# Kernel tuning notes

Measured on AMD Instinct MI355X. Metric: run time of the kernel, lower is better.

Reference implementation:

```python
import jax, jax.numpy as jnp
import numpy as np

HEAD_DIM = 64
N_HEADS = 32
N_KV = 8
ROPE_BASE = 500000.0
FREQ_CONFIG = {"factor": 32.0, "low_freq_factor": 1.0, "high_freq_factor": 4.0, "original_context_length": 8192}


def _rope_tables(head_dim, theta, n_pos, fc):
    # faithful to precompute_rope_params with llama3 freq scaling
    inv_freq = 1.0 / theta ** (np.arange(0, head_dim, 2, dtype=np.float32) / head_dim)
    low_wl = fc["original_context_length"] / fc["low_freq_factor"]
    high_wl = fc["original_context_length"] / fc["high_freq_factor"]
    wavelen = 2.0 * np.pi / inv_freq
    inv_l = np.where(wavelen > low_wl, inv_freq / fc["factor"], inv_freq)
    smooth = (fc["original_context_length"] / wavelen - fc["low_freq_factor"]) / (fc["high_freq_factor"] - fc["low_freq_factor"])
    smoothed = (1.0 - smooth) * (inv_freq / fc["factor"]) + smooth * inv_freq
    med = (wavelen <= low_wl) & (wavelen >= high_wl)
    inv_freq = np.where(med, smoothed, inv_l)
    pos = np.arange(n_pos, dtype=np.float32)
    angles = pos[:, None] * inv_freq[None, :]          # [T, head_dim/2]
    angles = np.concatenate([angles, angles], axis=1)  # [T, head_dim]
    return jnp.asarray(np.cos(angles), jnp.float32), jnp.asarray(np.sin(angles), jnp.float32)


def _apply_rope(x, cos, sin):
    # x: [b, h, t, d]; cos/sin: [t, d]
    d = x.shape[-1]
    x1, x2 = x[..., : d // 2], x[..., d // 2:]
    rotated = jnp.concatenate([-x2, x1], axis=-1)
    return x * cos[None, None] + rotated * sin[None, None]


def setup_inputs() -> dict:
    key = jax.random.key(0)
    ks = jax.random.split(key, 5)
    b, t, d = 1, 2048, 2048
    s = 0.02
    return {
        "x": jax.random.normal(ks[0], (b, t, d), jnp.float32),
        "Wq": jax.random.normal(ks[1], (d, d), jnp.float32) * s,
        "Wk": jax.random.normal(ks[2], (N_KV * HEAD_DIM, d), jnp.float32) * s,
        "Wv": jax.random.normal(ks[3], (N_KV * HEAD_DIM, d), jnp.float32) * s,
        "Wo": jax.random.normal(ks[4], (d, d), jnp.float32) * s,
        "start_pos": 0,
    }


def reference(x, Wq, Wk, Wv, Wo, start_pos):
    b, t, _ = x.shape
    cos, sin = _rope_tables(HEAD_DIM, ROPE_BASE, start_pos + t, FREQ_CONFIG)
    cos, sin = cos[start_pos:start_pos + t], sin[start_pos:start_pos + t]

    q = (x @ Wq.T).reshape(b, t, N_HEADS, HEAD_DIM).transpose(0, 2, 1, 3)  # [b,H,t,d]
    k = (x @ Wk.T).reshape(b, t, N_KV, HEAD_DIM).transpose(0, 2, 1, 3)     # [b,G,t,d]
    v = (x @ Wv.T).reshape(b, t, N_KV, HEAD_DIM).transpose(0, 2, 1, 3)

    q = _apply_rope(q, cos, sin)
    k = _apply_rope(k, cos, sin)

    n_rep = N_HEADS // N_KV
    k = jnp.repeat(k, n_rep, axis=1)  # [b,H,t,d]
    v = jnp.repeat(v, n_rep, axis=1)

    scores = jnp.einsum("bhqd,bhkd->bhqk", q, k)
    causal = jnp.triu(jnp.ones((t, t), bool), k=1)
    scores = jnp.where(causal[None, None], -jnp.inf, scores) / jnp.sqrt(jnp.float32(HEAD_DIM))
    weights = jax.nn.softmax(scores, axis=-1)
    ctx = jnp.einsum("bhqk,bhkd->bhqd", weights, v)
    ctx = ctx.transpose(0, 2, 1, 3).reshape(b, t, N_HEADS * HEAD_DIM)
    return ctx @ Wo.T
```

## Files before the change

### kernel.cpp

```cpp
#include <hip/hip_runtime.h>
#include <math.h>

#define T_SEQ 2048
#define D_MODEL 2048
#define HEAD_DIM 64
#define N_HEADS 32
#define N_KV 8

using short8 = __attribute__((ext_vector_type(8))) short;
using f32x4  = __attribute__((ext_vector_type(4))) float;
using f32x16 = __attribute__((ext_vector_type(16))) float;
using u32x4  = __attribute__((ext_vector_type(4))) unsigned int;

#define MFMA16(a, b, c) __builtin_amdgcn_mfma_f32_16x16x32_bf16(a, b, c, 0, 0, 0)
#define MFMA32(a, b, c) __builtin_amdgcn_mfma_f32_32x32x16_bf16(a, b, c, 0, 0, 0)

__device__ __forceinline__ unsigned short f2bf(float f) {
    unsigned int u = __builtin_bit_cast(unsigned int, f);
    u += 0x7fff + ((u >> 16) & 1);
    return (unsigned short)(u >> 16);
}
__device__ __forceinline__ void gld_lds16(const ushort* g, ushort* l) {
    __builtin_amdgcn_global_load_lds((const __attribute__((address_space(1))) void*)g,
                                     (__attribute__((address_space(3))) void*)l, 16, 0, 0);
}
__device__ __forceinline__ unsigned int cvtpk(float lo, float hi) {
    unsigned int r;
    asm("v_cvt_pk_bf16_f32 %0, %1, %2" : "=v"(r) : "v"(lo), "v"(hi));
    return r;
}
__device__ __forceinline__ void plswap(unsigned int& a, unsigned int& b) {
    auto r = __builtin_amdgcn_permlane32_swap(a, b, false, false);
    a = r[0];
    b = r[1];
}

__global__ __launch_bounds__(256) void rope_tables_kernel(float* __restrict__ cosT, float* __restrict__ sinT,
                                                          const int* __restrict__ start_pos, int T) {
    int idx = blockIdx.x * 256 + threadIdx.x;
    int t = idx >> 5;
    int i = idx & 31;
    float pos = (float)(start_pos[0] + t);
    float expo = (float)i / 32.0f;
    float inv_freq = 1.0f / powf(500000.0f, expo);
    const float two_pi = 6.283185307179586f;
    float wavelen = two_pi / inv_freq;
    const float low_wl = 8192.0f;
    const float high_wl = 2048.0f;
    float inv;
    if (wavelen > low_wl) {
        inv = inv_freq / 32.0f;
    } else if (wavelen < high_wl) {
        inv = inv_freq;
    } else {
        float smooth = (8192.0f / wavelen - 1.0f) / 3.0f;
        inv = (1.0f - smooth) * (inv_freq / 32.0f) + smooth * inv_freq;
    }
    float ang = pos * inv;
    cosT[i * T + t] = cosf(ang);
    sinT[i * T + t] = sinf(ang);
}

__global__ __launch_bounds__(256) void cast_all_kernel(
    const float* __restrict__ x, const float* __restrict__ wq,
    const float* __restrict__ wk, const float* __restrict__ wv,
    const float* __restrict__ wo,
    ushort* __restrict__ xb, ushort* __restrict__ wqb,
    ushort* __restrict__ wkb, ushort* __restrict__ wvb, ushort* __restrict__ wob) {
    int i = blockIdx.x * 256 + threadIdx.x;
    const float* src; ushort* dst; int off;
    if (i < 1048576)      { src = x;  dst = xb;  off = i; }
    else if (i < 2097152) { src = wq; dst = wqb; off = i - 1048576; }
    else if (i < 2359296) { src = wk; dst = wkb; off = i - 2097152; }
    else if (i < 2621440) { src = wv; dst = wvb; off = i - 2359296; }
    else                  { src = wo; dst = wob; off = i - 2621440; }
    float4 v = ((const float4*)src)[off];
    ushort4 o;
    o.x = f2bf(v.x); o.y = f2bf(v.y); o.z = f2bf(v.z); o.w = f2bf(v.w);
    ((ushort4*)dst)[off] = o;
}

__global__ __launch_bounds__(256) void gemm_qkv(
    const ushort* __restrict__ X, const ushort* __restrict__ Wqb,
    const ushort* __restrict__ Wkb, const ushort* __restrict__ Wvb,
    ushort* __restrict__ Qo, ushort* __restrict__ Ko, ushort* __restrict__ Vto,
    const float* __restrict__ cosT, const float* __restrict__ sinT,
    int T, int D) {
    __shared__ __align__(16) ushort As[2][2][2048];
    __shared__ __align__(16) ushort Bs[2][2][4096];
    const int tid = threadIdx.x;
    const int w = tid >> 6, l = tid & 63;
    const int m0 = blockIdx.x * 64;
    const int n0g = blockIdx.y * 128;

    const ushort* B;
    ushort* Cout;
    int n0, doRope;
    if (n0g < 2048)      { B = Wqb + (size_t)n0g * D;          Cout = Qo;  n0 = n0g;        doRope = 1; }
    else if (n0g < 2560) { B = Wkb + (size_t)(n0g - 2048) * D; Cout = Ko;  n0 = n0g - 2048; doRope = 1; }
    else                 { B = Wvb + (size_t)(n0g - 2560) * D; Cout = Vto; n0 = n0g - 2560; doRope = 0; }

    const int wm = (w >> 1) * 32, wn = (w & 1) * 64;
    const int lr = l & 15;
    const int quad = l >> 4;

    f32x4 zero = {0.f, 0.f, 0.f, 0.f};
    f32x4 acc[2][4];
#pragma unroll
    for (int i = 0; i < 2; ++i)
#pragma unroll
        for (int j = 0; j < 4; ++j) acc[i][j] = zero;

    const int srow = l >> 2;
    const int scg  = ((l & 3) ^ (srow & 3)) * 8;
    const ushort* Ag  = X + (size_t)(m0 + 16 * w + srow) * D + scg;
    const ushort* Bg0 = B + (size_t)(16 * (2 * w) + srow) * D + scg;
    const ushort* Bg1 = B + (size_t)(16 * (2 * w + 1) + srow) * D + scg;

#define GSTAGE(k0v, nb) { \
    gld_lds16(Ag  + (k0v),      &As[nb][0][w * 512]); \
    gld_lds16(Ag  + (k0v) + 32, &As[nb][1][w * 512]); \
    gld_lds16(Bg0 + (k0v),      &Bs[nb][0][(2 * w) * 512]); \
    gld_lds16(Bg0 + (k0v) + 32, &Bs[nb][1][(2 * w) * 512]); \
    gld_lds16(Bg1 + (k0v),      &Bs[nb][0][(2 * w + 1) * 512]); \
    gld_lds16(Bg1 + (k0v) + 32, &Bs[nb][1][(2 * w + 1) * 512]); }

    GSTAGE(0, 0);

    const int rsw = (quad ^ (lr & 3)) * 8;
    for (int k0 = 0; k0 < D; k0 += 64) {
        const int b = (k0 >> 6) & 1;
        __syncthreads();
        if (k0 + 64 < D) GSTAGE(k0 + 64, b ^ 1);
#pragma unroll
        for (int sub = 0; sub < 2; ++sub) {
            short8 af[2], bf[4];
#pragma unroll
            for (int i = 0; i < 2; ++i) af[i] = *(const short8*)&As[b][sub][(wm + i * 16 + lr) * 32 + rsw];
#pragma unroll
            for (int j = 0; j < 4; ++j) bf[j] = *(const short8*)&Bs[b][sub][(wn + j * 16 + lr) * 32 + rsw];
#pragma unroll
            for (int i = 0; i < 2; ++i)
#pragma unroll
                for (int j = 0; j < 4; ++j)
                    acc[i][j] = MFMA16(af[i], bf[j], acc[i][j]);
        }
    }
#undef GSTAGE

    const int mbase = m0 + wm + quad * 4;
    if (doRope) {
        const float qsc = (n0g < 2048) ? 0.18033688011112042f : 1.0f;
#pragma unroll
        for (int i = 0; i < 2; ++i) {
            int trow = mbase + i * 16;
#pragma unroll
            for (int j = 0; j < 2; ++j) {
                int i1 = lr + j * 16;
                float4 c4 = *(const float4*)&cosT[(size_t)i1 * T + trow];
                float4 s4 = *(const float4*)&sinT[(size_t)i1 * T + trow];
                int n1 = n0 + wn + lr + j * 16;
                int n2 = n1 + 32;
                size_t b1 = (size_t)(n1 >> 6) * ((size_t)T * 64) + (size_t)(n1 & 63);
                size_t b2 = (size_t)(n2 >> 6) * ((size_t)T * 64) + (size_t)(n2 & 63);
                float cs[4] = {c4.x, c4.y, c4.z, c4.w};
                float sn[4] = {s4.x, s4.y, s4.z, s4.w};
#pragma unroll
                for (int r = 0; r < 4; ++r) {
                    float x1 = acc[i][j][r], x2 = acc[i][j + 2][r];
                    Cout[b1 + (size_t)(trow + r) * 64] = f2bf((x1 * cs[r] - x2 * sn[r]) * qsc);
                    Cout[b2 + (size_t)(trow + r) * 64] = f2bf((x2 * cs[r] + x1 * sn[r]) * qsc);
                }
            }
        }
    } else {
#pragma unroll
        for (int i = 0; i < 2; ++i)
#pragma unroll
            for (int j = 0; j < 4; ++j) {
                int n = n0 + wn + lr + j * 16;
                int m = mbase + i * 16;
                ushort4 o;
                o.x = f2bf(acc[i][j][0]); o.y = f2bf(acc[i][j][1]);
                o.z = f2bf(acc[i][j][2]); o.w = f2bf(acc[i][j][3]);
                *(ushort4*)&Vto[(size_t)n * T + m] = o;
            }
    }
}

__global__ __launch_bounds__(256) void gemm_bt_f32(const ushort* __restrict__ A,
                                                   const ushort* __restrict__ B,
                                                   float* __restrict__ C,
                                                   int M, int N, int K) {
    __shared__ __align__(16) ushort As[2][2][2048];
    __shared__ __align__(16) ushort Bs[2][2][4096];
    const int tid = threadIdx.x;
    const int w = tid >> 6, l = tid & 63;
    const int m0 = blockIdx.x * 64, n0 = blockIdx.y * 128;
    const int wm = (w >> 1) * 32, wn = (w & 1) * 64;
    const int lr = l & 15;
    const int quad = l >> 4;

    f32x4 zero = {0.f, 0.f, 0.f, 0.f};
    f32x4 acc[2][4];
#pragma unroll
    for (int i = 0; i < 2; ++i)
#pragma unroll
        for (int j = 0; j < 4; ++j) acc[i][j] = zero;

    const int srow = l >> 2;
    const int scg  = ((l & 3) ^ (srow & 3)) * 8;
    const ushort* Ag  = A + (size_t)(m0 + 16 * w + srow) * K + scg;
    const ushort* Bg0 = B + (size_t)(n0 + 16 * (2 * w) + srow) * K + scg;
    const ushort* Bg1 = B + (size_t)(n0 + 16 * (2 * w + 1) + srow) * K + scg;

#define GSTAGE(k0v, nb) { \
    gld_lds16(Ag  + (k0v),      &As[nb][0][w * 512]); \
    gld_lds16(Ag  + (k0v) + 32, &As[nb][1][w * 512]); \
    gld_lds16(Bg0 + (k0v),      &Bs[nb][0][(2 * w) * 512]); \
    gld_lds16(Bg0 + (k0v) + 32, &Bs[nb][1][(2 * w) * 512]); \
    gld_lds16(Bg1 + (k0v),      &Bs[nb][0][(2 * w + 1) * 512]); \
    gld_lds16(Bg1 + (k0v) + 32, &Bs[nb][1][(2 * w + 1) * 512]); }

    GSTAGE(0, 0);

    const int rsw = (quad ^ (lr & 3)) * 8;
    for (int k0 = 0; k0 < K; k0 += 64) {
        const int b = (k0 >> 6) & 1;
        __syncthreads();
        if (k0 + 64 < K) GSTAGE(k0 + 64, b ^ 1);
#pragma unroll
        for (int sub = 0; sub < 2; ++sub) {
            short8 af[2], bf[4];
#pragma unroll
            for (int i = 0; i < 2; ++i) af[i] = *(const short8*)&As[b][sub][(wm + i * 16 + lr) * 32 + rsw];
#pragma unroll
            for (int j = 0; j < 4; ++j) bf[j] = *(const short8*)&Bs[b][sub][(wn + j * 16 + lr) * 32 + rsw];
#pragma unroll
            for (int i = 0; i < 2; ++i)
#pragma unroll
                for (int j = 0; j < 4; ++j)
                    acc[i][j] = MFMA16(af[i], bf[j], acc[i][j]);
        }
    }
#undef GSTAGE

    const int mbase = m0 + wm + quad * 4;
    const int nbase = n0 + wn + lr;
#pragma unroll
    for (int i = 0; i < 2; ++i)
#pragma unroll
        for (int j = 0; j < 4; ++j)
#pragma unroll
            for (int r = 0; r < 4; ++r)
                C[(size_t)(mbase + i * 16 + r) * N + (nbase + j * 16)] = acc[i][j][r];
}

__global__ __launch_bounds__(128, 2) void attn_mfma(const ushort* __restrict__ Q,
                                                    const ushort* __restrict__ K,
                                                    const ushort* __restrict__ Vt,
                                                    ushort* __restrict__ ctx, int T) {
    __shared__ __align__(16) ushort Ks[2][4096];
    __shared__ __align__(16) ushort Vs[2][4096];
    const int tid = threadIdx.x, w = tid >> 6, l = tid & 63;
    const int lq = l & 31, hi = l >> 5;
    const int h = blockIdx.y, hk = h >> 2;
    const int qb = ((h >> 3) & 1) ? (31 - (int)blockIdx.x) : (int)blockIdx.x;
    const int ntiles = qb + 1;
    const ushort* Kb = K + (size_t)hk * T * 64;
    const ushort* Vb = Vt + (size_t)hk * 64 * T;

    const int srow = l >> 3;
    const int sc   = ((l & 7) ^ srow) * 8;

    const ushort* Qrow = Q + ((size_t)h * T + qb * 64 + w * 32 + lq) * 64;
    short8 qf[4];
#pragma unroll
    for (int ks = 0; ks < 4; ++ks)
        qf[ks] = *(const short8*)(Qrow + ks * 16 + hi * 8);

    f32x16 oacc0, oacc1;
#pragma unroll
    for (int r = 0; r < 16; ++r) { oacc0[r] = 0.f; oacc1[r] = 0.f; }
    float ls[4] = {0.f, 0.f, 0.f, 0.f};
    const int limit = w * 32 + lq;

#define ASTAGE(kt, buf) do { \
    size_t _k0 = (size_t)(kt) * 64; \
    const int _s0 = w * 4; \
    gld_lds16(Kb + (_k0 + _s0 * 8      + srow) * 64 + sc, &Ks[buf][(_s0    ) * 512]); \
    gld_lds16(Kb + (_k0 + _s0 * 8 + 8  + srow) * 64 + sc, &Ks[buf][(_s0 + 1) * 512]); \
    gld_lds16(Kb + (_k0 + _s0 * 8 + 16 + srow) * 64 + sc, &Ks[buf][(_s0 + 2) * 512]); \
    gld_lds16(Kb + (_k0 + _s0 * 8 + 24 + srow) * 64 + sc, &Ks[buf][(_s0 + 3) * 512]); \
    gld_lds16(Vb + (size_t)(_s0 * 8      + srow) * T + _k0 + sc, &Vs[buf][(_s0    ) * 512]); \
    gld_lds16(Vb + (size_t)(_s0 * 8 + 8  + srow) * T + _k0 + sc, &Vs[buf][(_s0 + 1) * 512]); \
    gld_lds16(Vb + (size_t)(_s0 * 8 + 16 + srow) * T + _k0 + sc, &Vs[buf][(_s0 + 2) * 512]); \
    gld_lds16(Vb + (size_t)(_s0 * 8 + 24 + srow) * T + _k0 + sc, &Vs[buf][(_s0 + 3) * 512]); \
} while (0)

    ASTAGE(0, 0);

    for (int kt = 0; kt < ntiles; ++kt) {
        const int b = kt & 1;
        __syncthreads();
        if (kt + 1 < ntiles) ASTAGE(kt + 1, b ^ 1);

        f32x16 s0, s1;
#pragma unroll
        for (int r = 0; r < 16; ++r) { s0[r] = 0.f; s1[r] = 0.f; }
#pragma unroll
        for (int ks = 0; ks < 4; ++ks) {
            const int c = ((ks * 2 + hi) ^ (lq & 7)) * 8;
            short8 kf0 = *(const short8*)&Ks[b][lq * 64 + c];
            short8 kf1 = *(const short8*)&Ks[b][(lq + 32) * 64 + c];
            s0 = MFMA32(kf0, qf[ks], s0);
            s1 = MFMA32(kf1, qf[ks], s1);
        }

        f32x16 p0, p1;
        if (kt == ntiles - 1) {
#pragma unroll
            for (int r = 0; r < 16; ++r) {
                const int kk = (r & 3) + 8 * (r >> 2) + 4 * hi;
                p0[r] = (kk <= limit)      ? __builtin_amdgcn_exp2f(s0[r]) : 0.f;
                p1[r] = (kk + 32 <= limit) ? __builtin_amdgcn_exp2f(s1[r]) : 0.f;
            }
        } else {
#pragma unroll
            for (int r = 0; r < 16; ++r) {
                p0[r] = __builtin_amdgcn_exp2f(s0[r]);
                p1[r] = __builtin_amdgcn_exp2f(s1[r]);
            }
        }
#pragma unroll
        for (int r = 0; r < 16; ++r) ls[r & 3] += p0[r] + p1[r];

#pragma unroll
        for (int ks2 = 0; ks2 < 4; ++ks2) {
            const f32x16& pp = (ks2 < 2) ? p0 : p1;
            const int bse = (ks2 & 1) * 8;
            unsigned int a0 = cvtpk(pp[bse + 0], pp[bse + 1]);
            unsigned int a1 = cvtpk(pp[bse + 2], pp[bse + 3]);
            unsigned int b0 = cvtpk(pp[bse + 4], pp[bse + 5]);
            unsigned int b1 = cvtpk(pp[bse + 6], pp[bse + 7]);
            plswap(a0, b0);
            plswap(a1, b1);
            u32x4 tw = {a0, a1, b0, b1};
            short8 pf = __builtin_bit_cast(short8, tw);
            const int c = ((ks2 * 2 + hi) ^ (lq & 7)) * 8;
            short8 vf0 = *(const short8*)&Vs[b][lq * 64 + c];
            short8 vf1 = *(const short8*)&Vs[b][(lq + 32) * 64 + c];
            oacc0 = MFMA32(vf0, pf, oacc0);
            oacc1 = MFMA32(vf1, pf, oacc1);
        }
    }
#undef ASTAGE

    float vsum = (ls[0] + ls[1]) + (ls[2] + ls[3]);
    vsum += __shfl_xor(vsum, 32, 64);
    const float inv = 1.f / vsum;

    ushort* cp = ctx + (size_t)(qb * 64 + w * 32 + lq) * 2048 + h * 64;
#pragma unroll
    for (int g = 0; g < 4; ++g) {
        ushort4 o0, o1;
        o0.x = f2bf(oacc0[4 * g + 0] * inv); o0.y = f2bf(oacc0[4 * g + 1] * inv);
        o0.z = f2bf(oacc0[4 * g + 2] * inv); o0.w = f2bf(oacc0[4 * g + 3] * inv);
        *(ushort4*)&cp[g * 8 + hi * 4] = o0;
        o1.x = f2bf(oacc1[4 * g + 0] * inv); o1.y = f2bf(oacc1[4 * g + 1] * inv);
        o1.z = f2bf(oacc1[4 * g + 2] * inv); o1.w = f2bf(oacc1[4 * g + 3] * inv);
        *(ushort4*)&cp[32 + g * 8 + hi * 4] = o1;
    }
}

extern "C" void kernel_launch(void* const* d_in, const int* in_sizes, int n_in,
                              void* d_out, int out_size, void* d_ws, size_t ws_size,
                              hipStream_t stream) {
    const float* x  = (const float*)d_in[0];
    const float* Wq = (const float*)d_in[1];
    const float* Wk = (const float*)d_in[2];
    const float* Wv = (const float*)d_in[3];
    const float* Wo = (const float*)d_in[4];
    const int* start_pos = (const int*)d_in[5];
    float* out = (float*)d_out;

    const int T = T_SEQ, D = D_MODEL;
    const int KV = N_KV * HEAD_DIM;

    char* w = (char*)d_ws;
    float* cosT = (float*)w;            w += (size_t)32 * T * 4;
    float* sinT = (float*)w;            w += (size_t)32 * T * 4;
    ushort* xbf  = (ushort*)w;          w += (size_t)T * D * 2;
    ushort* wqbf = (ushort*)w;          w += (size_t)D * D * 2;
    ushort* wkbf = (ushort*)w;          w += (size_t)KV * D * 2;
    ushort* wvbf = (ushort*)w;          w += (size_t)KV * D * 2;
    ushort* wobf = (ushort*)w;          w += (size_t)D * D * 2;
    ushort* qbf  = (ushort*)w;          w += (size_t)N_HEADS * T * 64 * 2;
    ushort* kbf  = (ushort*)w;          w += (size_t)N_KV * T * 64 * 2;
    ushort* vtbf = (ushort*)w;          w += (size_t)N_KV * 64 * T * 2;
    ushort* ctxbf = xbf;

    rope_tables_kernel<<<dim3((T * 32) / 256), dim3(256), 0, stream>>>(cosT, sinT, start_pos, T);

    cast_all_kernel<<<dim3(14336), dim3(256), 0, stream>>>(x, Wq, Wk, Wv, Wo,
                                                           xbf, wqbf, wkbf, wvbf, wobf);

    gemm_qkv<<<dim3(T / 64, (D + 2 * KV) / 128), dim3(256), 0, stream>>>(
        xbf, wqbf, wkbf, wvbf, qbf, kbf, vtbf, cosT, sinT, T, D);

    attn_mfma<<<dim3(32, N_HEADS), dim3(128), 0, stream>>>(qbf, kbf, vtbf, ctxbf, T);

    gemm_bt_f32<<<dim3(T / 64, D / 128), dim3(256), 0, stream>>>(ctxbf, wobf, out, T, D, D);
}
```

Before: 205.4 us.

## Use single-wave attention blocks loading K/V directly from global memory

The attention kernel moves from two-wave blocks that share double-buffered LDS tiles of K/V to single-wave blocks of 32 query rows. Each wave reads K and V fragments straight from global memory (relying on cache) with no LDS and no barriers. It also skips the fully masked half of the last tile, launches blocks heaviest-first, and raises wave priority around the MFMA sections. The cost is twice as many global K/V fetches per query row and exposed load latency, since nothing is prefetched.

```diff
diff --git a/kernel.cpp b/kernel.cpp
--- a/kernel.cpp
+++ b/kernel.cpp
@@ -256,87 +256,86 @@
                 C[(size_t)(mbase + i * 16 + r) * N + (nbase + j * 16)] = acc[i][j][r];
 }
 
-__global__ __launch_bounds__(128, 2) void attn_mfma(const ushort* __restrict__ Q,
-                                                    const ushort* __restrict__ K,
-                                                    const ushort* __restrict__ Vt,
-                                                    ushort* __restrict__ ctx, int T) {
-    __shared__ __align__(16) ushort Ks[2][4096];
-    __shared__ __align__(16) ushort Vs[2][4096];
-    const int tid = threadIdx.x, w = tid >> 6, l = tid & 63;
+__global__ __launch_bounds__(64, 4) void attn_mfma(const ushort* __restrict__ Q,
+                                                   const ushort* __restrict__ K,
+                                                   const ushort* __restrict__ Vt,
+                                                   ushort* __restrict__ ctx, int T) {
+    const int l = threadIdx.x;
     const int lq = l & 31, hi = l >> 5;
     const int h = blockIdx.y, hk = h >> 2;
-    const int qb = ((h >> 3) & 1) ? (31 - (int)blockIdx.x) : (int)blockIdx.x;
-    const int ntiles = qb + 1;
+    const int qt = 63 - (int)blockIdx.x;
+    const int ntiles = qt / 2 + 1;
+    const int qrow = qt * 32 + lq;
     const ushort* Kb = K + (size_t)hk * T * 64;
     const ushort* Vb = Vt + (size_t)hk * 64 * T;
 
-    const int srow = l >> 3;
-    const int sc   = ((l & 7) ^ srow) * 8;
-
-    const ushort* Qrow = Q + ((size_t)h * T + qb * 64 + w * 32 + lq) * 64;
+    const ushort* Qrow = Q + ((size_t)h * T + qrow) * 64;
     short8 qf[4];
 #pragma unroll
     for (int ks = 0; ks < 4; ++ks)
         qf[ks] = *(const short8*)(Qrow + ks * 16 + hi * 8);
 
+    const ushort* Kl = Kb + (size_t)lq * 64 + hi * 8;
+    const ushort* Vl = Vb + (size_t)lq * T + hi * 8;
+
     f32x16 oacc0, oacc1;
 #pragma unroll
     for (int r = 0; r < 16; ++r) { oacc0[r] = 0.f; oacc1[r] = 0.f; }
     float ls[4] = {0.f, 0.f, 0.f, 0.f};
-    const int limit = w * 32 + lq;
-
-#define ASTAGE(kt, buf) do { \
-    size_t _k0 = (size_t)(kt) * 64; \
-    const int _s0 = w * 4; \
-    gld_lds16(Kb + (_k0 + _s0 * 8      + srow) * 64 + sc, &Ks[buf][(_s0    ) * 512]); \
-    gld_lds16(Kb + (_k0 + _s0 * 8 + 8  + srow) * 64 + sc, &Ks[buf][(_s0 + 1) * 512]); \
-    gld_lds16(Kb + (_k0 + _s0 * 8 + 16 + srow) * 64 + sc, &Ks[buf][(_s0 + 2) * 512]); \
-    gld_lds16(Kb + (_k0 + _s0 * 8 + 24 + srow) * 64 + sc, &Ks[buf][(_s0 + 3) * 512]); \
-    gld_lds16(Vb + (size_t)(_s0 * 8      + srow) * T + _k0 + sc, &Vs[buf][(_s0    ) * 512]); \
-    gld_lds16(Vb + (size_t)(_s0 * 8 + 8  + srow) * T + _k0 + sc, &Vs[buf][(_s0 + 1) * 512]); \
-    gld_lds16(Vb + (size_t)(_s0 * 8 + 16 + srow) * T + _k0 + sc, &Vs[buf][(_s0 + 2) * 512]); \
-    gld_lds16(Vb + (size_t)(_s0 * 8 + 24 + srow) * T + _k0 + sc, &Vs[buf][(_s0 + 3) * 512]); \
-} while (0)
-
-    ASTAGE(0, 0);
 
     for (int kt = 0; kt < ntiles; ++kt) {
-        const int b = kt & 1;
-        __syncthreads();
-        if (kt + 1 < ntiles) ASTAGE(kt + 1, b ^ 1);
+        const int k0 = kt * 64;
+        const bool last = (kt == ntiles - 1);
+        const bool halfT = last && ((qt & 1) == 0);
 
         f32x16 s0, s1;
 #pragma unroll
         for (int r = 0; r < 16; ++r) { s0[r] = 0.f; s1[r] = 0.f; }
+        __builtin_amdgcn_s_setprio(1);
 #pragma unroll
         for (int ks = 0; ks < 4; ++ks) {
-            const int c = ((ks * 2 + hi) ^ (lq & 7)) * 8;
-            short8 kf0 = *(const short8*)&Ks[b][lq * 64 + c];
-            short8 kf1 = *(const short8*)&Ks[b][(lq + 32) * 64 + c];
+            short8 kf0 = *(const short8*)(Kl + (size_t)(k0) * 64 + ks * 16);
             s0 = MFMA32(kf0, qf[ks], s0);
-            s1 = MFMA32(kf1, qf[ks], s1);
-        }
+        }
+        if (!halfT) {
+#pragma unroll
+            for (int ks = 0; ks < 4; ++ks) {
+                short8 kf1 = *(const short8*)(Kl + (size_t)(k0 + 32) * 64 + ks * 16);
+                s1 = MFMA32(kf1, qf[ks], s1);
+            }
+        }
+        __builtin_amdgcn_s_setprio(0);
 
         f32x16 p0, p1;
-        if (kt == ntiles - 1) {
+        if (last) {
 #pragma unroll
             for (int r = 0; r < 16; ++r) {
-                const int kk = (r & 3) + 8 * (r >> 2) + 4 * hi;
-                p0[r] = (kk <= limit)      ? __builtin_amdgcn_exp2f(s0[r]) : 0.f;
-                p1[r] = (kk + 32 <= limit) ? __builtin_amdgcn_exp2f(s1[r]) : 0.f;
+                const int kk = k0 + (r & 3) + 8 * (r >> 2) + 4 * hi;
+                p0[r] = (kk <= qrow) ? __builtin_amdgcn_exp2f(s0[r]) : 0.f;
+            }
+            if (!halfT) {
+#pragma unroll
+                for (int r = 0; r < 16; ++r) {
+                    const int kk = k0 + 32 + (r & 3) + 8 * (r >> 2) + 4 * hi;
+                    p1[r] = (kk <= qrow) ? __builtin_amdgcn_exp2f(s1[r]) : 0.f;
+                }
             }
         } else {
 #pragma unroll
-            for (int r = 0; r < 16; ++r) {
-                p0[r] = __builtin_amdgcn_exp2f(s0[r]);
-                p1[r] = __builtin_amdgcn_exp2f(s1[r]);
-            }
-        }
-#pragma unroll
-        for (int r = 0; r < 16; ++r) ls[r & 3] += p0[r] + p1[r];
-
-#pragma unroll
-        for (int ks2 = 0; ks2 < 4; ++ks2) {
+            for (int r = 0; r < 16; ++r) p0[r] = __builtin_amdgcn_exp2f(s0[r]);
+#pragma unroll
+            for (int r = 0; r < 16; ++r) p1[r] = __builtin_amdgcn_exp2f(s1[r]);
+        }
+#pragma unroll
+        for (int r = 0; r < 16; ++r) ls[r & 3] += p0[r];
+        if (!halfT) {
+#pragma unroll
+            for (int r = 0; r < 16; ++r) ls[r & 3] += p1[r];
+        }
+
+        const int nks2 = halfT ? 2 : 4;
+        __builtin_amdgcn_s_setprio(1);
+        for (int ks2 = 0; ks2 < nks2; ++ks2) {
             const f32x16& pp = (ks2 < 2) ? p0 : p1;
             const int bse = (ks2 & 1) * 8;
             unsigned int a0 = cvtpk(pp[bse + 0], pp[bse + 1]);
@@ -347,20 +346,19 @@
             plswap(a1, b1);
             u32x4 tw = {a0, a1, b0, b1};
             short8 pf = __builtin_bit_cast(short8, tw);
-            const int c = ((ks2 * 2 + hi) ^ (lq & 7)) * 8;
-            short8 vf0 = *(const short8*)&Vs[b][lq * 64 + c];
-            short8 vf1 = *(const short8*)&Vs[b][(lq + 32) * 64 + c];
+            short8 vf0 = *(const short8*)(Vl + k0 + ks2 * 16);
+            short8 vf1 = *(const short8*)(Vl + (size_t)32 * T + k0 + ks2 * 16);
             oacc0 = MFMA32(vf0, pf, oacc0);
             oacc1 = MFMA32(vf1, pf, oacc1);
         }
-    }
-#undef ASTAGE
+        __builtin_amdgcn_s_setprio(0);
+    }
 
     float vsum = (ls[0] + ls[1]) + (ls[2] + ls[3]);
     vsum += __shfl_xor(vsum, 32, 64);
     const float inv = 1.f / vsum;
 
-    ushort* cp = ctx + (size_t)(qb * 64 + w * 32 + lq) * 2048 + h * 64;
+    ushort* cp = ctx + (size_t)qrow * 2048 + h * 64;
 #pragma unroll
     for (int g = 0; g < 4; ++g) {
         ushort4 o0, o1;
@@ -408,7 +406,7 @@
     gemm_qkv<<<dim3(T / 64, (D + 2 * KV) / 128), dim3(256), 0, stream>>>(
         xbf, wqbf, wkbf, wvbf, qbf, kbf, vtbf, cosT, sinT, T, D);
 
-    attn_mfma<<<dim3(32, N_HEADS), dim3(128), 0, stream>>>(qbf, kbf, vtbf, ctxbf, T);
+    attn_mfma<<<dim3(64, N_HEADS), dim3(64), 0, stream>>>(qbf, kbf, vtbf, ctxbf, T);
 
     gemm_bt_f32<<<dim3(T / 64, D / 128), dim3(256), 0, stream>>>(ctxbf, wobf, out, T, D, D);
 }
```

Measured after the change: 290.3 us. 41.3% more time.

## Share KV tiles across head pairs in attention and fuse rope-table into cast kernel

Applied to the files above, without the earlier changes.

The attention kernel now runs 256-thread blocks that cover two query heads sharing one KV head, so each K/V tile staged in LDS serves both heads. It also stages two 64-key tiles per step, which halves the number of barriers. Causal masking on the last tile skips the upper half of the score and PV MFMAs for the first row group, and s_setprio is raised around the MFMA sections. Separately, the rope-table computation is folded into the cast kernel as extra blocks, which removes one launch. The cost is more LDS per block (32KB) and added control-flow complexity.

```diff
diff --git a/kernel.cpp b/kernel.cpp
--- a/kernel.cpp
+++ b/kernel.cpp
@@ -35,38 +35,37 @@
     b = r[1];
 }
 
-__global__ __launch_bounds__(256) void rope_tables_kernel(float* __restrict__ cosT, float* __restrict__ sinT,
-                                                          const int* __restrict__ start_pos, int T) {
-    int idx = blockIdx.x * 256 + threadIdx.x;
-    int t = idx >> 5;
-    int i = idx & 31;
-    float pos = (float)(start_pos[0] + t);
-    float expo = (float)i / 32.0f;
-    float inv_freq = 1.0f / powf(500000.0f, expo);
-    const float two_pi = 6.283185307179586f;
-    float wavelen = two_pi / inv_freq;
-    const float low_wl = 8192.0f;
-    const float high_wl = 2048.0f;
-    float inv;
-    if (wavelen > low_wl) {
-        inv = inv_freq / 32.0f;
-    } else if (wavelen < high_wl) {
-        inv = inv_freq;
-    } else {
-        float smooth = (8192.0f / wavelen - 1.0f) / 3.0f;
-        inv = (1.0f - smooth) * (inv_freq / 32.0f) + smooth * inv_freq;
-    }
-    float ang = pos * inv;
-    cosT[i * T + t] = cosf(ang);
-    sinT[i * T + t] = sinf(ang);
-}
-
-__global__ __launch_bounds__(256) void cast_all_kernel(
+__global__ __launch_bounds__(256) void cast_rope_kernel(
     const float* __restrict__ x, const float* __restrict__ wq,
     const float* __restrict__ wk, const float* __restrict__ wv,
     const float* __restrict__ wo,
     ushort* __restrict__ xb, ushort* __restrict__ wqb,
-    ushort* __restrict__ wkb, ushort* __restrict__ wvb, ushort* __restrict__ wob) {
+    ushort* __restrict__ wkb, ushort* __restrict__ wvb, ushort* __restrict__ wob,
+    float* __restrict__ cosT, float* __restrict__ sinT,
+    const int* __restrict__ start_pos, int T) {
+    if (blockIdx.x >= 14336) {
+        int idx = (blockIdx.x - 14336) * 256 + threadIdx.x;
+        int t = idx >> 5;
+        int i = idx & 31;
+        float pos = (float)(start_pos[0] + t);
+        float expo = (float)i / 32.0f;
+        float inv_freq = 1.0f / powf(500000.0f, expo);
+        const float two_pi = 6.283185307179586f;
+        float wavelen = two_pi / inv_freq;
+        float inv;
+        if (wavelen > 8192.0f) {
+            inv = inv_freq / 32.0f;
+        } else if (wavelen < 2048.0f) {
+            inv = inv_freq;
+        } else {
+            float smooth = (8192.0f / wavelen - 1.0f) / 3.0f;
+            inv = (1.0f - smooth) * (inv_freq / 32.0f) + smooth * inv_freq;
+        }
+        float ang = pos * inv;
+        cosT[i * T + t] = cosf(ang);
+        sinT[i * T + t] = sinf(ang);
+        return;
+    }
     int i = blockIdx.x * 256 + threadIdx.x;
     const float* src; ushort* dst; int off;
     if (i < 1048576)      { src = x;  dst = xb;  off = i; }
@@ -256,24 +255,31 @@
                 C[(size_t)(mbase + i * 16 + r) * N + (nbase + j * 16)] = acc[i][j][r];
 }
 
-__global__ __launch_bounds__(128, 2) void attn_mfma(const ushort* __restrict__ Q,
+__global__ __launch_bounds__(256, 2) void attn_mfma(const ushort* __restrict__ Q,
                                                     const ushort* __restrict__ K,
                                                     const ushort* __restrict__ Vt,
                                                     ushort* __restrict__ ctx, int T) {
-    __shared__ __align__(16) ushort Ks[2][4096];
-    __shared__ __align__(16) ushort Vs[2][4096];
+    __shared__ __align__(16) ushort Ks[2][2][4096];
+    __shared__ __align__(16) ushort Vs[2][2][4096];
     const int tid = threadIdx.x, w = tid >> 6, l = tid & 63;
     const int lq = l & 31, hi = l >> 5;
-    const int h = blockIdx.y, hk = h >> 2;
-    const int qb = ((h >> 3) & 1) ? (31 - (int)blockIdx.x) : (int)blockIdx.x;
-    const int ntiles = qb + 1;
+    const int hp = blockIdx.y;
+    const int hk = hp >> 1;
+    const int h  = 2 * hp + (w & 1);
+    const int roff = (w >> 1) * 32;
+    const int bx = blockIdx.x;
+    const int qt = ((hp >> 3) & 1) ? (31 - bx) : bx;
+    const int nsteps = (qt + 2) >> 1;
+    const int qbase = qt * 64;
+    const int base = qbase + roff;
+    const int qrow = base + lq;
     const ushort* Kb = K + (size_t)hk * T * 64;
     const ushort* Vb = Vt + (size_t)hk * 64 * T;
 
     const int srow = l >> 3;
     const int sc   = ((l & 7) ^ srow) * 8;
 
-    const ushort* Qrow = Q + ((size_t)h * T + qb * 64 + w * 32 + lq) * 64;
+    const ushort* Qrow = Q + ((size_t)h * T + qrow) * 64;
     short8 qf[4];
 #pragma unroll
     for (int ks = 0; ks < 4; ++ks)
@@ -283,84 +289,113 @@
 #pragma unroll
     for (int r = 0; r < 16; ++r) { oacc0[r] = 0.f; oacc1[r] = 0.f; }
     float ls[4] = {0.f, 0.f, 0.f, 0.f};
-    const int limit = w * 32 + lq;
-
-#define ASTAGE(kt, buf) do { \
-    size_t _k0 = (size_t)(kt) * 64; \
-    const int _s0 = w * 4; \
-    gld_lds16(Kb + (_k0 + _s0 * 8      + srow) * 64 + sc, &Ks[buf][(_s0    ) * 512]); \
-    gld_lds16(Kb + (_k0 + _s0 * 8 + 8  + srow) * 64 + sc, &Ks[buf][(_s0 + 1) * 512]); \
-    gld_lds16(Kb + (_k0 + _s0 * 8 + 16 + srow) * 64 + sc, &Ks[buf][(_s0 + 2) * 512]); \
-    gld_lds16(Kb + (_k0 + _s0 * 8 + 24 + srow) * 64 + sc, &Ks[buf][(_s0 + 3) * 512]); \
-    gld_lds16(Vb + (size_t)(_s0 * 8      + srow) * T + _k0 + sc, &Vs[buf][(_s0    ) * 512]); \
-    gld_lds16(Vb + (size_t)(_s0 * 8 + 8  + srow) * T + _k0 + sc, &Vs[buf][(_s0 + 1) * 512]); \
-    gld_lds16(Vb + (size_t)(_s0 * 8 + 16 + srow) * T + _k0 + sc, &Vs[buf][(_s0 + 2) * 512]); \
-    gld_lds16(Vb + (size_t)(_s0 * 8 + 24 + srow) * T + _k0 + sc, &Vs[buf][(_s0 + 3) * 512]); \
+
+#define ASTAGE(t, buf, half) do { \
+    size_t _k0 = (size_t)(t) * 64; \
+    const int _c0 = 2 * w, _c1 = 2 * w + 1; \
+    gld_lds16(Kb + (_k0 + _c0 * 8 + srow) * 64 + sc, &Ks[buf][half][_c0 * 512]); \
+    gld_lds16(Kb + (_k0 + _c1 * 8 + srow) * 64 + sc, &Ks[buf][half][_c1 * 512]); \
+    gld_lds16(Vb + (size_t)(_c0 * 8 + srow) * T + _k0 + sc, &Vs[buf][half][_c0 * 512]); \
+    gld_lds16(Vb + (size_t)(_c1 * 8 + srow) * T + _k0 + sc, &Vs[buf][half][_c1 * 512]); \
 } while (0)
 
-    ASTAGE(0, 0);
-
-    for (int kt = 0; kt < ntiles; ++kt) {
-        const int b = kt & 1;
+#define CTILE(t, bb, hh) do { \
+    const bool lastg = ((t) == qt); \
+    const bool halfT = lastg && (roff == 0);    \
+    f32x16 s0, s1; \
+    _Pragma("unroll") \
+    for (int r = 0; r < 16; ++r) { s0[r] = 0.f; s1[r] = 0.f; } \
+    __builtin_amdgcn_s_setprio(1); \
+    _Pragma("unroll") \
+    for (int ks = 0; ks < 4; ++ks) { \
+        const int cc = ((ks * 2 + hi) ^ (lq & 7)) * 8; \
+        short8 kf0 = *(const short8*)&Ks[bb][hh][lq * 64 + cc]; \
+        s0 = MFMA32(kf0, qf[ks], s0); \
+    } \
+    if (!halfT) { \
+        _Pragma("unroll") \
+        for (int ks = 0; ks < 4; ++ks) { \
+            const int cc = ((ks * 2 + hi) ^ (lq & 7)) * 8; \
+            short8 kf1 = *(const short8*)&Ks[bb][hh][(lq + 32) * 64 + cc]; \
+            s1 = MFMA32(kf1, qf[ks], s1); \
+        } \
+    } \
+    __builtin_amdgcn_s_setprio(0); \
+    const int k0 = (t) * 64; \
+    if (lastg) { \
+        if (roff == 0) { \
+            _Pragma("unroll") \
+            for (int r = 0; r < 16; ++r) { \
+                const int kk = k0 + (r & 3) + 8 * (r >> 2) + 4 * hi; \
+                s0[r] = (kk <= qrow) ? __builtin_amdgcn_exp2f(s0[r]) : 0.f; \
+            } \
+        } else { \
+            _Pragma("unroll") \
+            for (int r = 0; r < 16; ++r) s0[r] = __builtin_amdgcn_exp2f(s0[r]); \
+            _Pragma("unroll") \
+            for (int r = 0; r < 16; ++r) { \
+                const int kk = k0 + 32 + (r & 3) + 8 * (r >> 2) + 4 * hi; \
+                s1[r] = (kk <= qrow) ? __builtin_amdgcn_exp2f(s1[r]) : 0.f; \
+            } \
+        } \
+    } else { \
+        _Pragma("unroll") \
+        for (int r = 0; r < 16; ++r) s0[r] = __builtin_amdgcn_exp2f(s0[r]); \
+        _Pragma("unroll") \
+        for (int r = 0; r < 16; ++r) s1[r] = __builtin_amdgcn_exp2f(s1[r]); \
+    } \
+    _Pragma("unroll") \
+    for (int r = 0; r < 16; ++r) ls[r & 3] += s0[r]; \
+    if (!halfT) { \
+        _Pragma("unroll") \
+        for (int r = 0; r < 16; ++r) ls[r & 3] += s1[r]; \
+    } \
+    const int nks2 = halfT ? 2 : 4; \
+    __builtin_amdgcn_s_setprio(1); \
+    for (int ks2 = 0; ks2 < nks2; ++ks2) { \
+        const f32x16& pp = (ks2 < 2) ? s0 : s1; \
+        const int bse = (ks2 & 1) * 8; \
+        unsigned int a0 = cvtpk(pp[bse + 0], pp[bse + 1]); \
+        unsigned int a1 = cvtpk(pp[bse + 2], pp[bse + 3]); \
+        unsigned int b0 = cvtpk(pp[bse + 4], pp[bse + 5]); \
+        unsigned int b1 = cvtpk(pp[bse + 6], pp[bse + 7]); \
+        plswap(a0, b0); \
+        plswap(a1, b1); \
+        u32x4 tw = {a0, a1, b0, b1}; \
+        short8 pf = __builtin_bit_cast(short8, tw); \
+        const int cc = ((ks2 * 2 + hi) ^ (lq & 7)) * 8; \
+        short8 vf0 = *(const short8*)&Vs[bb][hh][lq * 64 + cc]; \
+        short8 vf1 = *(const short8*)&Vs[bb][hh][(lq + 32) * 64 + cc]; \
+        oacc0 = MFMA32(vf0, pf, oacc0); \
+        oacc1 = MFMA32(vf1, pf, oacc1); \
+    } \
+    __builtin_amdgcn_s_setprio(0); \
+} while (0)
+
+    ASTAGE(0, 0, 0);
+    ASTAGE(1, 0, 1);
+
+    for (int s = 0; s < nsteps; ++s) {
+        const int b = s & 1;
         __syncthreads();
-        if (kt + 1 < ntiles) ASTAGE(kt + 1, b ^ 1);
-
-        f32x16 s0, s1;
-#pragma unroll
-        for (int r = 0; r < 16; ++r) { s0[r] = 0.f; s1[r] = 0.f; }
-#pragma unroll
-        for (int ks = 0; ks < 4; ++ks) {
-            const int c = ((ks * 2 + hi) ^ (lq & 7)) * 8;
-            short8 kf0 = *(const short8*)&Ks[b][lq * 64 + c];
-            short8 kf1 = *(const short8*)&Ks[b][(lq + 32) * 64 + c];
-            s0 = MFMA32(kf0, qf[ks], s0);
-            s1 = MFMA32(kf1, qf[ks], s1);
-        }
-
-        f32x16 p0, p1;
-        if (kt == ntiles - 1) {
-#pragma unroll
-            for (int r = 0; r < 16; ++r) {
-                const int kk = (r & 3) + 8 * (r >> 2) + 4 * hi;
-                p0[r] = (kk <= limit)      ? __builtin_amdgcn_exp2f(s0[r]) : 0.f;
-                p1[r] = (kk + 32 <= limit) ? __builtin_amdgcn_exp2f(s1[r]) : 0.f;
-            }
-        } else {
-#pragma unroll
-            for (int r = 0; r < 16; ++r) {
-                p0[r] = __builtin_amdgcn_exp2f(s0[r]);
-                p1[r] = __builtin_amdgcn_exp2f(s1[r]);
-            }
-        }
-#pragma unroll
-        for (int r = 0; r < 16; ++r) ls[r & 3] += p0[r] + p1[r];
-
-#pragma unroll
-        for (int ks2 = 0; ks2 < 4; ++ks2) {
-            const f32x16& pp = (ks2 < 2) ? p0 : p1;
-            const int bse = (ks2 & 1) * 8;
-            unsigned int a0 = cvtpk(pp[bse + 0], pp[bse + 1]);
-            unsigned int a1 = cvtpk(pp[bse + 2], pp[bse + 3]);
-            unsigned int b0 = cvtpk(pp[bse + 4], pp[bse + 5]);
-            unsigned int b1 = cvtpk(pp[bse + 6], pp[bse + 7]);
-            plswap(a0, b0);
-            plswap(a1, b1);
-            u32x4 tw = {a0, a1, b0, b1};
-            short8 pf = __builtin_bit_cast(short8, tw);
-            const int c = ((ks2 * 2 + hi) ^ (lq & 7)) * 8;
-            short8 vf0 = *(const short8*)&Vs[b][lq * 64 + c];
-            short8 vf1 = *(const short8*)&Vs[b][(lq + 32) * 64 + c];
-            oacc0 = MFMA32(vf0, pf, oacc0);
-            oacc1 = MFMA32(vf1, pf, oacc1);
-        }
-    }
+        if (s + 1 < nsteps) {
+            ASTAGE(2 * s + 2, b ^ 1, 0);
+            ASTAGE(2 * s + 3, b ^ 1, 1);
+        }
+        CTILE(2 * s, b, 0);
+        const int t1 = 2 * s + 1;
+        if (t1 * 64 <= base + 31) {
+            CTILE(t1, b, 1);
+        }
+    }
+#undef CTILE
 #undef ASTAGE
 
     float vsum = (ls[0] + ls[1]) + (ls[2] + ls[3]);
     vsum += __shfl_xor(vsum, 32, 64);
     const float inv = 1.f / vsum;
 
-    ushort* cp = ctx + (size_t)(qb * 64 + w * 32 + lq) * 2048 + h * 64;
+    ushort* cp = ctx + (size_t)qrow * 2048 + h * 64;
 #pragma unroll
     for (int g = 0; g < 4; ++g) {
         ushort4 o0, o1;
@@ -400,15 +435,13 @@
     ushort* vtbf = (ushort*)w;          w += (size_t)N_KV * 64 * T * 2;
     ushort* ctxbf = xbf;
 
-    rope_tables_kernel<<<dim3((T * 32) / 256), dim3(256), 0, stream>>>(cosT, sinT, start_pos, T);
-
-    cast_all_kernel<<<dim3(14336), dim3(256), 0, stream>>>(x, Wq, Wk, Wv, Wo,
-                                                           xbf, wqbf, wkbf, wvbf, wobf);
+    cast_rope_kernel<<<dim3(14336 + 256), dim3(256), 0, stream>>>(
+        x, Wq, Wk, Wv, Wo, xbf, wqbf, wkbf, wvbf, wobf, cosT, sinT, start_pos, T);
 
     gemm_qkv<<<dim3(T / 64, (D + 2 * KV) / 128), dim3(256), 0, stream>>>(
         xbf, wqbf, wkbf, wvbf, qbf, kbf, vtbf, cosT, sinT, T, D);
 
-    attn_mfma<<<dim3(32, N_HEADS), dim3(128), 0, stream>>>(qbf, kbf, vtbf, ctxbf, T);
+    attn_mfma<<<dim3(32, 16), dim3(256), 0, stream>>>(qbf, kbf, vtbf, ctxbf, T);
 
     gemm_bt_f32<<<dim3(T / 64, D / 128), dim3(256), 0, stream>>>(ctxbf, wobf, out, T, D, D);
 }
```

After: 202.7 us. No clear change (-1.3%).
